# Performance work log

Measured on AMD Instinct MI355X. Metric: run time of the kernel, lower is better.

Reference implementation:

```python
import jax, jax.numpy as jnp
import numpy as np

NEG = 1e12  # matches the torch '-inf' surrogate value


def _sinusoidal_pos(seq_len, dim):
    # bert4keras-style: pe[..., 0::2] = sin, pe[..., 1::2] = cos
    pos = jnp.arange(seq_len, dtype=jnp.float32)
    i = jnp.arange(dim // 2, dtype=jnp.float32)
    freq = jnp.power(10000.0, -2.0 * i / dim)
    ang = pos[:, None] * freq[None, :]                      # [S, dim/2]
    pe = jnp.stack([jnp.sin(ang), jnp.cos(ang)], axis=-1)   # [S, dim/2, 2]
    return pe.reshape(seq_len, dim)                          # [S, dim]


def _rope(e, cos_pos, sin_pos):
    # additional_part = stack([-e[...,1::2], e[...,::2]], -1).reshape(e.shape)
    rot = jnp.stack([-e[..., 1::2], e[..., 0::2]], axis=-1).reshape(e.shape)
    return e * cos_pos + rot * sin_pos


def setup_inputs() -> dict:
    key = jax.random.key(0)
    k = jax.random.split(key, 5)
    B, S, H, inner, L = 8, 512, 768, 64, 16
    x = jax.random.normal(k[0], (B, S, H), dtype=jnp.float32)
    W1 = jax.random.normal(k[1], (H, 2 * inner), dtype=jnp.float32) * 0.02
    b1 = jnp.zeros((2 * inner,), dtype=jnp.float32)
    W2 = jax.random.normal(k[2], (H, 2 * L), dtype=jnp.float32) * 0.02
    b2 = jnp.zeros((2 * L,), dtype=jnp.float32)
    attention_mask = jnp.ones((B, S), dtype=jnp.int32)
    return {"x": x, "W1": W1, "b1": b1, "W2": W2, "b2": b2,
            "attention_mask": attention_mask}


def reference(x, W1, b1, W2, b2, attention_mask):
    B, S, H = x.shape
    inner = W1.shape[1] // 2

    t = x @ W1 + b1                                 # [B,S,2*inner]
    start_token = t[..., 0::2]                      # [B,S,inner]
    end_token = t[..., 1::2]                        # [B,S,inner]

    pe = _sinusoidal_pos(S, inner)[None]            # [1,S,inner]
    cos_pos = jnp.repeat(pe[..., 1::2], 2, axis=-1)
    sin_pos = jnp.repeat(pe[..., 0::2], 2, axis=-1)
    start_token = _rope(start_token, cos_pos, sin_pos)
    end_token = _rope(end_token, cos_pos, sin_pos)

    span_score = jnp.einsum('bmd,bnd->bmn', start_token, end_token) / (inner ** 0.5)

    typing = jnp.swapaxes(x @ W2 + b2, 1, 2) / 2.0  # [B,2L,S]

    # entity_score: [B, L, S(start), S(end)]
    entity_score = (span_score[:, None]
                    + typing[:, 0::2, None, :]
                    + typing[:, 1::2, :, None])

    m = attention_mask.astype(entity_score.dtype)
    m_row = m[:, None, :, None]                     # mask over start axis
    m_col = m[:, None, None, :]                     # mask over end axis
    entity_score = entity_score * m_row + (-NEG) * (1.0 - m_row)
    entity_score = entity_score * m_col + (-NEG) * (1.0 - m_col)

    tril = jnp.tril(jnp.ones((S, S), entity_score.dtype), k=-1)
    entity_score = entity_score - tril * NEG
    return entity_score
```

## Files before the change

kernel.cpp:

```cpp
#include <hip/hip_runtime.h>

#define NEGF 1.0e12f

constexpr int Hdim = 768;
constexpr int NC   = 160;
constexpr int ROWS = 4096;
constexpr int SEQ  = 512;
constexpr int KSPLIT = 4;

typedef __attribute__((ext_vector_type(8))) short  short8;
typedef __attribute__((ext_vector_type(4))) float  floatx4;

__device__ inline unsigned short f2bf(float f) {
    union { float f; unsigned u; } v; v.f = f;
    return (unsigned short)((v.u + 0x8000u) >> 16);
}

__global__ __launch_bounds__(256) void gemm_mfma_k(
    const float* __restrict__ x, const float* __restrict__ W1,
    const float* __restrict__ W2, float* __restrict__ partial)
{
    __shared__ __align__(16) unsigned short xs[64 * 40];
    __shared__ __align__(16) unsigned short ws[NC * 40];

    const int tid  = threadIdx.x;
    const int wave = tid >> 6;
    const int lane = tid & 63;
    const int quad = lane >> 4;
    const int nl   = lane & 15;
    const int r0   = blockIdx.x * 64;
    const int k0   = blockIdx.y * 192;

    floatx4 acc[10];
#pragma unroll
    for (int t = 0; t < 10; t++) acc[t] = (floatx4)(0.0f);

    for (int kt = 0; kt < 192; kt += 32) {
        const int kb = k0 + kt;
        {
            const int row = tid >> 2;
            const int kq  = (tid & 3) * 8;
            const float* xp = x + (size_t)(r0 + row) * Hdim + kb + kq;
            float4 v0 = *(const float4*)xp;
            float4 v1 = *(const float4*)(xp + 4);
            short8 sv;
            sv[0] = (short)f2bf(v0.x); sv[1] = (short)f2bf(v0.y);
            sv[2] = (short)f2bf(v0.z); sv[3] = (short)f2bf(v0.w);
            sv[4] = (short)f2bf(v1.x); sv[5] = (short)f2bf(v1.y);
            sv[6] = (short)f2bf(v1.z); sv[7] = (short)f2bf(v1.w);
            *(short8*)(xs + row * 40 + kq) = sv;
        }
#pragma unroll
        for (int g = 0; g < 3; g++) {
            const int c   = g * 64 + (tid & 63);
            const int kq2 = (tid >> 6) * 8;
            if (c < NC) {
                float f[8];
                if (c < 128) {
                    const float* wp = W1 + (size_t)(kb + kq2) * 128 + c;
#pragma unroll
                    for (int j = 0; j < 8; j++) f[j] = wp[j * 128];
                } else {
                    const float* wp = W2 + (size_t)(kb + kq2) * 32 + (c - 128);
#pragma unroll
                    for (int j = 0; j < 8; j++) f[j] = wp[j * 32];
                }
                short8 sv;
#pragma unroll
                for (int j = 0; j < 8; j++) sv[j] = (short)f2bf(f[j]);
                *(short8*)(ws + c * 40 + kq2) = sv;
            }
        }
        __syncthreads();

        short8 af = *(const short8*)(xs + (wave * 16 + nl) * 40 + quad * 8);
#pragma unroll
        for (int t = 0; t < 10; t++) {
            short8 bf = *(const short8*)(ws + (t * 16 + nl) * 40 + quad * 8);
            acc[t] = __builtin_amdgcn_mfma_f32_16x16x32_bf16(af, bf, acc[t], 0, 0, 0);
        }
        __syncthreads();
    }

    float* pout = partial + (size_t)blockIdx.y * ROWS * NC;
#pragma unroll
    for (int t = 0; t < 10; t++) {
#pragma unroll
        for (int r = 0; r < 4; r++) {
            pout[(size_t)(r0 + wave * 16 + quad * 4 + r) * NC + t * 16 + nl] = acc[t][r];
        }
    }
}

__global__ __launch_bounds__(256) void combine_rope_k(
    const float* __restrict__ partial, const float* __restrict__ b1,
    const float* __restrict__ b2, unsigned short* __restrict__ startbf,
    unsigned short* __restrict__ endbf, float* __restrict__ tyn,
    float* __restrict__ tym)
{
    const int tid = threadIdx.x;
    const int row = blockIdx.x * 4 + (tid >> 6);
    const int u   = tid & 63;
    const int b   = row >> 9;
    const int s   = row & 511;
    const float* p0 = partial + (size_t)row * NC;
    const size_t cstride = (size_t)ROWS * NC;

    if (u < 32) {
        const int i = u;
        float4 a0 = *(const float4*)(p0 + 4 * i);
        float4 a1 = *(const float4*)(p0 + cstride + 4 * i);
        float4 a2 = *(const float4*)(p0 + 2 * cstride + 4 * i);
        float4 a3 = *(const float4*)(p0 + 3 * cstride + 4 * i);
        float t0 = a0.x + a1.x + a2.x + a3.x + b1[4 * i + 0];
        float t1 = a0.y + a1.y + a2.y + a3.y + b1[4 * i + 1];
        float t2 = a0.z + a1.z + a2.z + a3.z + b1[4 * i + 2];
        float t3 = a0.w + a1.w + a2.w + a3.w + b1[4 * i + 3];
        float freq = __powf(10000.0f, -(float)i * (1.0f / 32.0f));
        float ang  = (float)s * freq;
        float sn, cs;
        __sincosf(ang, &sn, &cs);
        float so0 = (t0 * cs - t2 * sn) * 0.125f;
        float so1 = (t2 * cs + t0 * sn) * 0.125f;
        float eo0 = t1 * cs - t3 * sn;
        float eo1 = t3 * cs + t1 * sn;
        ushort2 sp; sp.x = f2bf(so0); sp.y = f2bf(so1);
        ushort2 ep; ep.x = f2bf(eo0); ep.y = f2bf(eo1);
        *(ushort2*)(startbf + (size_t)row * 64 + 2 * i) = sp;
        *(ushort2*)(endbf   + (size_t)row * 64 + 2 * i) = ep;
    } else {
        const int j = u - 32;
        float t = p0[128 + j] + p0[cstride + 128 + j] + p0[2 * cstride + 128 + j]
                + p0[3 * cstride + 128 + j] + b2[j];
        float v = t * 0.5f;
        const int l = j >> 1;
        if ((j & 1) == 0) tyn[((size_t)b * 16 + l) * SEQ + s] = v;
        else              tym[((size_t)b * 16 + l) * SEQ + s] = v;
    }
}

__global__ __launch_bounds__(256) void entity_k(
    const unsigned short* __restrict__ startbf, const unsigned short* __restrict__ endbf,
    const float* __restrict__ tyn, const float* __restrict__ tym,
    const int* __restrict__ amask, float* __restrict__ out)
{
    __shared__ __align__(16) unsigned short sA[64 * 72];
    __shared__ __align__(16) unsigned short sB[64 * 72];
    __shared__ float tyn_s[16 * 64];
    __shared__ float tym_s[16 * 64];
    __shared__ float mrow_s[64];
    __shared__ float mcol_s[64];

    const int tid = threadIdx.x;
    const int b   = blockIdx.z;
    const int m0  = blockIdx.y * 64;
    const int n0  = blockIdx.x * 64;

    for (int t = tid; t < 512; t += 256) {
        int row = t >> 3;
        int kq  = (t & 7) * 8;
        *(short8*)(sA + row * 72 + kq) =
            *(const short8*)(startbf + (size_t)(b * SEQ + m0 + row) * 64 + kq);
        *(short8*)(sB + row * 72 + kq) =
            *(const short8*)(endbf + (size_t)(b * SEQ + n0 + row) * 64 + kq);
    }
    for (int t = tid; t < 16 * 64; t += 256) {
        int l = t >> 6, i = t & 63;
        tym_s[t] = tym[((size_t)b * 16 + l) * SEQ + m0 + i];
        tyn_s[t] = tyn[((size_t)b * 16 + l) * SEQ + n0 + i];
    }
    if (tid < 64)       mrow_s[tid] = (float)amask[b * SEQ + m0 + tid];
    else if (tid < 128) mcol_s[tid - 64] = (float)amask[b * SEQ + n0 + (tid - 64)];
    __syncthreads();

    const int wave = tid >> 6;
    const int lane = tid & 63;
    const int quad = lane >> 4;
    const int nl   = lane & 15;

    short8 a0 = *(const short8*)(sA + (wave * 16 + nl) * 72 + quad * 8);
    short8 a1 = *(const short8*)(sA + (wave * 16 + nl) * 72 + 32 + quad * 8);

    floatx4 acc[4];
#pragma unroll
    for (int t = 0; t < 4; t++) acc[t] = (floatx4)(0.0f);
#pragma unroll
    for (int t = 0; t < 4; t++) {
        short8 bf0 = *(const short8*)(sB + (t * 16 + nl) * 72 + quad * 8);
        short8 bf1 = *(const short8*)(sB + (t * 16 + nl) * 72 + 32 + quad * 8);
        acc[t] = __builtin_amdgcn_mfma_f32_16x16x32_bf16(a0, bf0, acc[t], 0, 0, 0);
        acc[t] = __builtin_amdgcn_mfma_f32_16x16x32_bf16(a1, bf1, acc[t], 0, 0, 0);
    }

    float mr[4], radd[4];
#pragma unroll
    for (int r = 0; r < 4; r++) {
        mr[r]   = mrow_s[wave * 16 + quad * 4 + r];
        radd[r] = -NEGF * (1.0f - mr[r]);
    }
    float mc[4], cadd[4];
#pragma unroll
    for (int t = 0; t < 4; t++) {
        mc[t]   = mcol_s[t * 16 + nl];
        cadd[t] = -NEGF * (1.0f - mc[t]);
    }
    const bool lower = (m0 > n0);
    const bool diag  = (m0 == n0);
    const int  lm    = wave * 16 + quad * 4;

    for (int l = 0; l < 16; l++) {
        float tmv[4];
#pragma unroll
        for (int r = 0; r < 4; r++) tmv[r] = tym_s[l * 64 + lm + r];
        float* ob = out + ((size_t)(b * 16 + l) * SEQ + m0 + lm) * SEQ + n0;
#pragma unroll
        for (int t = 0; t < 4; t++) {
            float tnv = tyn_s[l * 64 + t * 16 + nl];
#pragma unroll
            for (int r = 0; r < 4; r++) {
                float v = acc[t][r] + tnv + tmv[r];
                v = v * mr[r] + radd[r];
                v = v * mc[t] + cadd[t];
                if (lower) v -= NEGF;
                else if (diag && (lm + r > t * 16 + nl)) v -= NEGF;
                ob[(size_t)r * SEQ + t * 16 + nl] = v;
            }
        }
    }
}

extern "C" void kernel_launch(void* const* d_in, const int* in_sizes, int n_in,
                              void* d_out, int out_size, void* d_ws, size_t ws_size,
                              hipStream_t stream) {
    const float* x     = (const float*)d_in[0];
    const float* W1    = (const float*)d_in[1];
    const float* b1    = (const float*)d_in[2];
    const float* W2    = (const float*)d_in[3];
    const float* b2    = (const float*)d_in[4];
    const int*   amask = (const int*)d_in[5];
    float* out = (float*)d_out;

    char* base = (char*)d_ws;
    float*          partial = (float*)base;
    unsigned short* startbf = (unsigned short*)(base + 10485760);
    unsigned short* endbf   = (unsigned short*)(base + 10485760 + 524288);
    float*          tyn     = (float*)(base + 10485760 + 2 * 524288);
    float*          tym     = (float*)(base + 10485760 + 2 * 524288 + 262144);

    hipLaunchKernelGGL(gemm_mfma_k, dim3(64, KSPLIT), dim3(256), 0, stream,
                       x, W1, W2, partial);
    hipLaunchKernelGGL(combine_rope_k, dim3(ROWS / 4), dim3(256), 0, stream,
                       partial, b1, b2, startbf, endbf, tyn, tym);
    hipLaunchKernelGGL(entity_k, dim3(8, 8, 8), dim3(256), 0, stream,
                       startbf, endbf, tyn, tym, amask, out);
}
```

Before: 169.7 us.

## Transpose entity MFMA tile for float4 nontemporal stores, split labels, skip lower tiles

The entity kernel swaps the MFMA operand roles so each lane holds four consecutive output columns, which lets it write each group with one 16-byte nontemporal store instead of four scalar stores. The grid is doubled so each block handles 8 of the 16 labels, and blocks whose tile lies entirely below the diagonal skip the shared-memory loads and the MFMA. The aim is to cut store-instruction count and cache pollution on this write-bound output. In exchange, each block now reloads the same operand tiles for its half of the labels, and the transposed layout makes the masking and index logic more involved.

```diff
diff --git a/kernel.cpp b/kernel.cpp
--- a/kernel.cpp
+++ b/kernel.cpp
@@ -144,87 +144,95 @@
     const float* __restrict__ tyn, const float* __restrict__ tym,
     const int* __restrict__ amask, float* __restrict__ out)
 {
-    __shared__ __align__(16) unsigned short sA[64 * 72];
-    __shared__ __align__(16) unsigned short sB[64 * 72];
-    __shared__ float tyn_s[16 * 64];
-    __shared__ float tym_s[16 * 64];
+    __shared__ __align__(16) unsigned short sE[64 * 72];
+    __shared__ __align__(16) unsigned short sS[64 * 72];
+    __shared__ float tyn_s[8 * 64];
+    __shared__ float tym_s[8 * 64];
     __shared__ float mrow_s[64];
     __shared__ float mcol_s[64];
 
     const int tid = threadIdx.x;
-    const int b   = blockIdx.z;
+    const int bz  = blockIdx.z;
+    const int b   = bz >> 1;
+    const int l0  = (bz & 1) * 8;
     const int m0  = blockIdx.y * 64;
     const int n0  = blockIdx.x * 64;
-
-    for (int t = tid; t < 512; t += 256) {
-        int row = t >> 3;
-        int kq  = (t & 7) * 8;
-        *(short8*)(sA + row * 72 + kq) =
-            *(const short8*)(startbf + (size_t)(b * SEQ + m0 + row) * 64 + kq);
-        *(short8*)(sB + row * 72 + kq) =
-            *(const short8*)(endbf + (size_t)(b * SEQ + n0 + row) * 64 + kq);
-    }
-    for (int t = tid; t < 16 * 64; t += 256) {
-        int l = t >> 6, i = t & 63;
-        tym_s[t] = tym[((size_t)b * 16 + l) * SEQ + m0 + i];
-        tyn_s[t] = tyn[((size_t)b * 16 + l) * SEQ + n0 + i];
-    }
-    if (tid < 64)       mrow_s[tid] = (float)amask[b * SEQ + m0 + tid];
-    else if (tid < 128) mcol_s[tid - 64] = (float)amask[b * SEQ + n0 + (tid - 64)];
-    __syncthreads();
-
-    const int wave = tid >> 6;
-    const int lane = tid & 63;
-    const int quad = lane >> 4;
-    const int nl   = lane & 15;
-
-    short8 a0 = *(const short8*)(sA + (wave * 16 + nl) * 72 + quad * 8);
-    short8 a1 = *(const short8*)(sA + (wave * 16 + nl) * 72 + 32 + quad * 8);
-
-    floatx4 acc[4];
-#pragma unroll
-    for (int t = 0; t < 4; t++) acc[t] = (floatx4)(0.0f);
-#pragma unroll
-    for (int t = 0; t < 4; t++) {
-        short8 bf0 = *(const short8*)(sB + (t * 16 + nl) * 72 + quad * 8);
-        short8 bf1 = *(const short8*)(sB + (t * 16 + nl) * 72 + 32 + quad * 8);
-        acc[t] = __builtin_amdgcn_mfma_f32_16x16x32_bf16(a0, bf0, acc[t], 0, 0, 0);
-        acc[t] = __builtin_amdgcn_mfma_f32_16x16x32_bf16(a1, bf1, acc[t], 0, 0, 0);
-    }
-
-    float mr[4], radd[4];
-#pragma unroll
-    for (int r = 0; r < 4; r++) {
-        mr[r]   = mrow_s[wave * 16 + quad * 4 + r];
-        radd[r] = -NEGF * (1.0f - mr[r]);
-    }
-    float mc[4], cadd[4];
-#pragma unroll
-    for (int t = 0; t < 4; t++) {
-        mc[t]   = mcol_s[t * 16 + nl];
-        cadd[t] = -NEGF * (1.0f - mc[t]);
-    }
     const bool lower = (m0 > n0);
     const bool diag  = (m0 == n0);
-    const int  lm    = wave * 16 + quad * 4;
-
-    for (int l = 0; l < 16; l++) {
-        float tmv[4];
-#pragma unroll
-        for (int r = 0; r < 4; r++) tmv[r] = tym_s[l * 64 + lm + r];
-        float* ob = out + ((size_t)(b * 16 + l) * SEQ + m0 + lm) * SEQ + n0;
+
+    if (tid < 64)       mrow_s[tid]      = (float)amask[b * SEQ + m0 + tid];
+    else if (tid < 128) mcol_s[tid - 64] = (float)amask[b * SEQ + n0 + (tid - 64)];
+
+    if (!lower) {
+        for (int t = tid; t < 512; t += 256) {
+            int row = t >> 3;
+            int kq  = (t & 7) * 8;
+            *(short8*)(sE + row * 72 + kq) =
+                *(const short8*)(endbf + (size_t)(b * SEQ + n0 + row) * 64 + kq);
+            *(short8*)(sS + row * 72 + kq) =
+                *(const short8*)(startbf + (size_t)(b * SEQ + m0 + row) * 64 + kq);
+        }
+        for (int t = tid; t < 8 * 64; t += 256) {
+            int l = t >> 6, i = t & 63;
+            tym_s[t] = tym[((size_t)b * 16 + l0 + l) * SEQ + m0 + i];
+            tyn_s[t] = tyn[((size_t)b * 16 + l0 + l) * SEQ + n0 + i];
+        }
+    }
+    __syncthreads();
+
+    const int wave  = tid >> 6;
+    const int lane  = tid & 63;
+    const int quad  = lane >> 4;
+    const int nl    = lane & 15;
+    const int nloc0 = wave * 16 + quad * 4;
+
+    floatx4 acc[4];
+#pragma unroll
+    for (int t = 0; t < 4; t++) acc[t] = (floatx4)(0.0f);
+
+    if (!lower) {
+        short8 a0 = *(const short8*)(sE + (wave * 16 + nl) * 72 + quad * 8);
+        short8 a1 = *(const short8*)(sE + (wave * 16 + nl) * 72 + 32 + quad * 8);
 #pragma unroll
         for (int t = 0; t < 4; t++) {
-            float tnv = tyn_s[l * 64 + t * 16 + nl];
+            short8 bf0 = *(const short8*)(sS + (t * 16 + nl) * 72 + quad * 8);
+            short8 bf1 = *(const short8*)(sS + (t * 16 + nl) * 72 + 32 + quad * 8);
+            acc[t] = __builtin_amdgcn_mfma_f32_16x16x32_bf16(a0, bf0, acc[t], 0, 0, 0);
+            acc[t] = __builtin_amdgcn_mfma_f32_16x16x32_bf16(a1, bf1, acc[t], 0, 0, 0);
+        }
+    }
+
+    float mc4[4], cadd4[4];
+#pragma unroll
+    for (int r = 0; r < 4; r++) {
+        mc4[r]   = mcol_s[nloc0 + r];
+        cadd4[r] = -NEGF * (1.0f - mc4[r]);
+    }
+    float mrt[4], raddt[4];
+#pragma unroll
+    for (int t = 0; t < 4; t++) {
+        mrt[t]   = mrow_s[t * 16 + nl];
+        raddt[t] = -NEGF * (1.0f - mrt[t]);
+    }
+
+    for (int l = 0; l < 8; l++) {
+        floatx4 tn4 = (floatx4)(0.0f);
+        if (!lower) tn4 = *(const floatx4*)(tyn_s + l * 64 + nloc0);
+        float* op = out + (((size_t)(b * 16 + l0 + l)) * SEQ + m0) * SEQ + n0 + nloc0;
+#pragma unroll
+        for (int t = 0; t < 4; t++) {
+            float tm = lower ? 0.0f : tym_s[l * 64 + t * 16 + nl];
+            floatx4 v;
 #pragma unroll
             for (int r = 0; r < 4; r++) {
-                float v = acc[t][r] + tnv + tmv[r];
-                v = v * mr[r] + radd[r];
-                v = v * mc[t] + cadd[t];
-                if (lower) v -= NEGF;
-                else if (diag && (lm + r > t * 16 + nl)) v -= NEGF;
-                ob[(size_t)r * SEQ + t * 16 + nl] = v;
+                float x = acc[t][r] + tn4[r] + tm;
+                x = x * mrt[t] + raddt[t];
+                x = x * mc4[r] + cadd4[r];
+                if (lower) x -= NEGF;
+                else if (diag && (t * 16 + nl) > (nloc0 + r)) x -= NEGF;
+                v[r] = x;
             }
+            __builtin_nontemporal_store(v, (floatx4*)(op + (size_t)(t * 16 + nl) * SEQ));
         }
     }
 }
@@ -251,6 +259,6 @@
                        x, W1, W2, partial);
     hipLaunchKernelGGL(combine_rope_k, dim3(ROWS / 4), dim3(256), 0, stream,
                        partial, b1, b2, startbf, endbf, tyn, tym);
-    hipLaunchKernelGGL(entity_k, dim3(8, 8, 8), dim3(256), 0, stream,
+    hipLaunchKernelGGL(entity_k, dim3(8, 8, 16), dim3(256), 0, stream,
                        startbf, endbf, tyn, tym, amask, out);
 }
```

Result: slower. 190.5 us (+12.3%).

## Split entity kernel into span GEMM and vectorized broadcast-write kernel

Applied to the files above, without the earlier changes.

Splits the fused entity kernel into two. span_k computes only the upper-triangular span tiles and writes them to a workspace buffer that reuses the partial area. bcast_k then reads each span row once and writes all 16 label planes with contiguous float4 stores, zeroing the lower-triangular span terms before applying masks. The goal is to replace the strided scalar output stores of the old kernel with coalesced vector writes, at the cost of an extra launch and a round trip of the span matrix through memory.

```diff
diff --git a/kernel.cpp b/kernel.cpp
--- a/kernel.cpp
+++ b/kernel.cpp
@@ -139,23 +139,19 @@
     }
 }
 
-__global__ __launch_bounds__(256) void entity_k(
+__global__ __launch_bounds__(256) void span_k(
     const unsigned short* __restrict__ startbf, const unsigned short* __restrict__ endbf,
-    const float* __restrict__ tyn, const float* __restrict__ tym,
-    const int* __restrict__ amask, float* __restrict__ out)
-{
+    float* __restrict__ span)
+{
+    const int b  = blockIdx.z;
+    const int m0 = blockIdx.y * 64;
+    const int n0 = blockIdx.x * 64;
+    if (m0 > n0) return;
+
     __shared__ __align__(16) unsigned short sA[64 * 72];
     __shared__ __align__(16) unsigned short sB[64 * 72];
-    __shared__ float tyn_s[16 * 64];
-    __shared__ float tym_s[16 * 64];
-    __shared__ float mrow_s[64];
-    __shared__ float mcol_s[64];
 
     const int tid = threadIdx.x;
-    const int b   = blockIdx.z;
-    const int m0  = blockIdx.y * 64;
-    const int n0  = blockIdx.x * 64;
-
     for (int t = tid; t < 512; t += 256) {
         int row = t >> 3;
         int kq  = (t & 7) * 8;
@@ -164,13 +160,6 @@
         *(short8*)(sB + row * 72 + kq) =
             *(const short8*)(endbf + (size_t)(b * SEQ + n0 + row) * 64 + kq);
     }
-    for (int t = tid; t < 16 * 64; t += 256) {
-        int l = t >> 6, i = t & 63;
-        tym_s[t] = tym[((size_t)b * 16 + l) * SEQ + m0 + i];
-        tyn_s[t] = tyn[((size_t)b * 16 + l) * SEQ + n0 + i];
-    }
-    if (tid < 64)       mrow_s[tid] = (float)amask[b * SEQ + m0 + tid];
-    else if (tid < 128) mcol_s[tid - 64] = (float)amask[b * SEQ + n0 + (tid - 64)];
     __syncthreads();
 
     const int wave = tid >> 6;
@@ -192,39 +181,76 @@
         acc[t] = __builtin_amdgcn_mfma_f32_16x16x32_bf16(a1, bf1, acc[t], 0, 0, 0);
     }
 
-    float mr[4], radd[4];
-#pragma unroll
-    for (int r = 0; r < 4; r++) {
-        mr[r]   = mrow_s[wave * 16 + quad * 4 + r];
-        radd[r] = -NEGF * (1.0f - mr[r]);
-    }
-    float mc[4], cadd[4];
 #pragma unroll
     for (int t = 0; t < 4; t++) {
-        mc[t]   = mcol_s[t * 16 + nl];
-        cadd[t] = -NEGF * (1.0f - mc[t]);
-    }
-    const bool lower = (m0 > n0);
-    const bool diag  = (m0 == n0);
-    const int  lm    = wave * 16 + quad * 4;
-
-    for (int l = 0; l < 16; l++) {
-        float tmv[4];
-#pragma unroll
-        for (int r = 0; r < 4; r++) tmv[r] = tym_s[l * 64 + lm + r];
-        float* ob = out + ((size_t)(b * 16 + l) * SEQ + m0 + lm) * SEQ + n0;
-#pragma unroll
-        for (int t = 0; t < 4; t++) {
-            float tnv = tyn_s[l * 64 + t * 16 + nl];
-#pragma unroll
-            for (int r = 0; r < 4; r++) {
-                float v = acc[t][r] + tnv + tmv[r];
-                v = v * mr[r] + radd[r];
-                v = v * mc[t] + cadd[t];
-                if (lower) v -= NEGF;
-                else if (diag && (lm + r > t * 16 + nl)) v -= NEGF;
-                ob[(size_t)r * SEQ + t * 16 + nl] = v;
+#pragma unroll
+        for (int r = 0; r < 4; r++) {
+            span[((size_t)(b * SEQ) + m0 + wave * 16 + quad * 4 + r) * SEQ
+                 + n0 + t * 16 + nl] = acc[t][r];
+        }
+    }
+}
+
+__global__ __launch_bounds__(256) void bcast_k(
+    const float* __restrict__ span, const float* __restrict__ tyn,
+    const float* __restrict__ tym, const int* __restrict__ amask,
+    float* __restrict__ out)
+{
+    __shared__ float tyn_s[8 * SEQ];
+    __shared__ float tym_s[64];
+
+    const int tid = threadIdx.x;
+    const int m0  = blockIdx.x * 8;
+    const int l0  = blockIdx.y * 8;
+    const int b   = blockIdx.z;
+
+    for (int t = tid; t < 8 * SEQ / 4; t += 256)
+        ((floatx4*)tyn_s)[t] = ((const floatx4*)(tyn + ((size_t)b * 16 + l0) * SEQ))[t];
+    if (tid < 64) {
+        int l = tid >> 3, r = tid & 7;
+        tym_s[tid] = tym[((size_t)b * 16 + l0 + l) * SEQ + m0 + r];
+    }
+
+    const int r  = tid >> 5;
+    const int cb = (tid & 31) * 4;
+    const int m  = m0 + r;
+    const float mr   = (float)amask[b * SEQ + m];
+    const float radd = -NEGF * (1.0f - mr);
+
+    float spanz[16], mc[16], cadd2[16];
+#pragma unroll
+    for (int q = 0; q < 4; q++) {
+        floatx4 s4 = *(const floatx4*)(span + ((size_t)b * SEQ + m) * SEQ + cb + q * 128);
+        int4 mk = *(const int4*)(amask + b * SEQ + cb + q * 128);
+        const int* mki = (const int*)&mk;
+#pragma unroll
+        for (int e = 0; e < 4; e++) {
+            const int j = q * 4 + e;
+            const int n = cb + q * 128 + e;
+            mc[j] = (float)mki[e];
+            float ca = -NEGF * (1.0f - mc[j]);
+            cadd2[j] = (n < m) ? (ca - NEGF) : ca;
+            spanz[j] = (n >= m) ? s4[e] : 0.0f;
+        }
+    }
+    __syncthreads();
+
+    for (int l = 0; l < 8; l++) {
+        const float tm = tym_s[l * 8 + r];
+        float* orow = out + (((size_t)(b * 16 + l0 + l)) * SEQ + m) * SEQ;
+#pragma unroll
+        for (int q = 0; q < 4; q++) {
+            floatx4 t4 = *(const floatx4*)(tyn_s + l * SEQ + cb + q * 128);
+            floatx4 v;
+#pragma unroll
+            for (int e = 0; e < 4; e++) {
+                const int j = q * 4 + e;
+                float x = spanz[j] + t4[e] + tm;
+                x = x * mr + radd;
+                x = x * mc[j] + cadd2[j];
+                v[e] = x;
             }
+            *(floatx4*)(orow + cb + q * 128) = v;
         }
     }
 }
@@ -246,11 +272,14 @@
     unsigned short* endbf   = (unsigned short*)(base + 10485760 + 524288);
     float*          tyn     = (float*)(base + 10485760 + 2 * 524288);
     float*          tym     = (float*)(base + 10485760 + 2 * 524288 + 262144);
+    float*          span    = partial;
 
     hipLaunchKernelGGL(gemm_mfma_k, dim3(64, KSPLIT), dim3(256), 0, stream,
                        x, W1, W2, partial);
     hipLaunchKernelGGL(combine_rope_k, dim3(ROWS / 4), dim3(256), 0, stream,
                        partial, b1, b2, startbf, endbf, tyn, tym);
-    hipLaunchKernelGGL(entity_k, dim3(8, 8, 8), dim3(256), 0, stream,
-                       startbf, endbf, tyn, tym, amask, out);
-}
+    hipLaunchKernelGGL(span_k, dim3(8, 8, 8), dim3(256), 0, stream,
+                       startbf, endbf, span);
+    hipLaunchKernelGGL(bcast_k, dim3(64, 2, 8), dim3(256), 0, stream,
+                       span, tyn, tym, amask, out);
+}
```

After: 175.3 us. 1.03x slower.

## Fuse split-K GEMM with RoPE combine and restructure entity kernel by row strips

Applied to the files above, without the earlier changes.

The projection GEMM now does its K-split inside one block, with two wave pairs each covering half of K. Their partials are reduced through shared memory and RoPE plus typing are applied in the same kernel. This removes the global partial buffer and the separate combine launch. The entity kernel now computes a 16-row by full-512-column span strip per block, skips MFMA tiles entirely below the diagonal, and stages typing in LDS. It then writes 8 labels with float4 row-contiguous stores. In exchange the GEMM runs on only 256 blocks, and the entity kernel carries more registers and LDS per block.

```diff
diff --git a/kernel.cpp b/kernel.cpp
--- a/kernel.cpp
+++ b/kernel.cpp
@@ -3,12 +3,10 @@
 #define NEGF 1.0e12f
 
 constexpr int Hdim = 768;
-constexpr int NC   = 160;
-constexpr int ROWS = 4096;
 constexpr int SEQ  = 512;
-constexpr int KSPLIT = 4;
 
 typedef __attribute__((ext_vector_type(8))) short  short8;
+typedef __attribute__((ext_vector_type(4))) short  short4v;
 typedef __attribute__((ext_vector_type(4))) float  floatx4;
 
 __device__ inline unsigned short f2bf(float f) {
@@ -16,106 +14,108 @@
     return (unsigned short)((v.u + 0x8000u) >> 16);
 }
 
-__global__ __launch_bounds__(256) void gemm_mfma_k(
+__global__ __launch_bounds__(256) void gemm_rope_k(
     const float* __restrict__ x, const float* __restrict__ W1,
-    const float* __restrict__ W2, float* __restrict__ partial)
+    const float* __restrict__ W2, const float* __restrict__ b1,
+    const float* __restrict__ b2, unsigned short* __restrict__ startbf,
+    unsigned short* __restrict__ endbf, float* __restrict__ tyn,
+    float* __restrict__ tym)
 {
-    __shared__ __align__(16) unsigned short xs[64 * 40];
-    __shared__ __align__(16) unsigned short ws[NC * 40];
+    __shared__ __align__(16) char smem[28160];
+    unsigned short* xs = (unsigned short*)smem;
+    unsigned short* ws = xs + 2 * 16 * 40;
+    float* tacc = (float*)smem;
 
     const int tid  = threadIdx.x;
+    const int r0   = blockIdx.x * 16;
     const int wave = tid >> 6;
     const int lane = tid & 63;
     const int quad = lane >> 4;
     const int nl   = lane & 15;
-    const int r0   = blockIdx.x * 64;
-    const int k0   = blockIdx.y * 192;
-
-    floatx4 acc[10];
-#pragma unroll
-    for (int t = 0; t < 10; t++) acc[t] = (floatx4)(0.0f);
-
-    for (int kt = 0; kt < 192; kt += 32) {
-        const int kb = k0 + kt;
+    const int ch   = wave & 1;
+    const int kh   = wave >> 1;
+
+    floatx4 acc[5];
+#pragma unroll
+    for (int t = 0; t < 5; t++) acc[t] = (floatx4)(0.0f);
+
+    for (int kt = 0; kt < 384; kt += 32) {
         {
-            const int row = tid >> 2;
-            const int kq  = (tid & 3) * 8;
-            const float* xp = x + (size_t)(r0 + row) * Hdim + kb + kq;
-            float4 v0 = *(const float4*)xp;
-            float4 v1 = *(const float4*)(xp + 4);
-            short8 sv;
-            sv[0] = (short)f2bf(v0.x); sv[1] = (short)f2bf(v0.y);
-            sv[2] = (short)f2bf(v0.z); sv[3] = (short)f2bf(v0.w);
-            sv[4] = (short)f2bf(v1.x); sv[5] = (short)f2bf(v1.y);
-            sv[6] = (short)f2bf(v1.z); sv[7] = (short)f2bf(v1.w);
-            *(short8*)(xs + row * 40 + kq) = sv;
-        }
-#pragma unroll
-        for (int g = 0; g < 3; g++) {
-            const int c   = g * 64 + (tid & 63);
-            const int kq2 = (tid >> 6) * 8;
-            if (c < NC) {
-                float f[8];
-                if (c < 128) {
-                    const float* wp = W1 + (size_t)(kb + kq2) * 128 + c;
-#pragma unroll
-                    for (int j = 0; j < 8; j++) f[j] = wp[j * 128];
-                } else {
-                    const float* wp = W2 + (size_t)(kb + kq2) * 32 + (c - 128);
-#pragma unroll
-                    for (int j = 0; j < 8; j++) f[j] = wp[j * 32];
+            const int khs = tid >> 7;
+            const int row = (tid >> 3) & 15;
+            const int kq  = (tid & 7) * 4;
+            const float* xp = x + (size_t)(r0 + row) * Hdim + khs * 384 + kt + kq;
+            float4 v = *(const float4*)xp;
+            short4v sv;
+            sv[0] = (short)f2bf(v.x); sv[1] = (short)f2bf(v.y);
+            sv[2] = (short)f2bf(v.z); sv[3] = (short)f2bf(v.w);
+            *(short4v*)(xs + khs * 640 + row * 40 + kq) = sv;
+        }
+        {
+            const int khs = tid >> 7;
+            const int sub = tid & 127;
+            const int kq2 = (sub >> 6) * 8;
+#pragma unroll
+            for (int g = 0; g < 3; g++) {
+                const int c = g * 64 + (sub & 63);
+                if (c < 160) {
+#pragma unroll
+                    for (int h = 0; h < 2; h++) {
+                        const int ko = kq2 + h * 16;
+                        const int kg = khs * 384 + kt + ko;
+                        float f[8];
+                        if (c < 128) {
+                            const float* wp = W1 + (size_t)kg * 128 + c;
+#pragma unroll
+                            for (int j = 0; j < 8; j++) f[j] = wp[j * 128];
+                        } else {
+                            const float* wp = W2 + (size_t)kg * 32 + (c - 128);
+#pragma unroll
+                            for (int j = 0; j < 8; j++) f[j] = wp[j * 32];
+                        }
+                        short8 sv;
+#pragma unroll
+                        for (int j = 0; j < 8; j++) sv[j] = (short)f2bf(f[j]);
+                        *(short8*)(ws + khs * 6400 + c * 40 + ko) = sv;
+                    }
                 }
-                short8 sv;
-#pragma unroll
-                for (int j = 0; j < 8; j++) sv[j] = (short)f2bf(f[j]);
-                *(short8*)(ws + c * 40 + kq2) = sv;
             }
         }
         __syncthreads();
 
-        short8 af = *(const short8*)(xs + (wave * 16 + nl) * 40 + quad * 8);
-#pragma unroll
-        for (int t = 0; t < 10; t++) {
-            short8 bf = *(const short8*)(ws + (t * 16 + nl) * 40 + quad * 8);
+        short8 af = *(const short8*)(xs + kh * 640 + nl * 40 + quad * 8);
+#pragma unroll
+        for (int t = 0; t < 5; t++) {
+            short8 bf = *(const short8*)(ws + kh * 6400 + (ch * 80 + t * 16 + nl) * 40 + quad * 8);
             acc[t] = __builtin_amdgcn_mfma_f32_16x16x32_bf16(af, bf, acc[t], 0, 0, 0);
         }
         __syncthreads();
     }
 
-    float* pout = partial + (size_t)blockIdx.y * ROWS * NC;
-#pragma unroll
-    for (int t = 0; t < 10; t++) {
-#pragma unroll
-        for (int r = 0; r < 4; r++) {
-            pout[(size_t)(r0 + wave * 16 + quad * 4 + r) * NC + t * 16 + nl] = acc[t][r];
-        }
-    }
-}
-
-__global__ __launch_bounds__(256) void combine_rope_k(
-    const float* __restrict__ partial, const float* __restrict__ b1,
-    const float* __restrict__ b2, unsigned short* __restrict__ startbf,
-    unsigned short* __restrict__ endbf, float* __restrict__ tyn,
-    float* __restrict__ tym)
-{
-    const int tid = threadIdx.x;
-    const int row = blockIdx.x * 4 + (tid >> 6);
-    const int u   = tid & 63;
-    const int b   = row >> 9;
-    const int s   = row & 511;
-    const float* p0 = partial + (size_t)row * NC;
-    const size_t cstride = (size_t)ROWS * NC;
-
-    if (u < 32) {
-        const int i = u;
-        float4 a0 = *(const float4*)(p0 + 4 * i);
-        float4 a1 = *(const float4*)(p0 + cstride + 4 * i);
-        float4 a2 = *(const float4*)(p0 + 2 * cstride + 4 * i);
-        float4 a3 = *(const float4*)(p0 + 3 * cstride + 4 * i);
-        float t0 = a0.x + a1.x + a2.x + a3.x + b1[4 * i + 0];
-        float t1 = a0.y + a1.y + a2.y + a3.y + b1[4 * i + 1];
-        float t2 = a0.z + a1.z + a2.z + a3.z + b1[4 * i + 2];
-        float t3 = a0.w + a1.w + a2.w + a3.w + b1[4 * i + 3];
+#pragma unroll
+    for (int t = 0; t < 5; t++)
+#pragma unroll
+        for (int r = 0; r < 4; r++)
+            tacc[kh * (16 * 164) + (quad * 4 + r) * 164 + ch * 80 + t * 16 + nl] = acc[t][r];
+    __syncthreads();
+
+    const int row = tid >> 4;
+    const int uu  = tid & 15;
+    const int R   = r0 + row;
+    const int bb  = R >> 9;
+    const int s   = R & 511;
+    const float* t0p = tacc + row * 164;
+    const float* t1p = tacc + 16 * 164 + row * 164;
+#pragma unroll
+    for (int ii = 0; ii < 2; ii++) {
+        const int i = uu + ii * 16;
+        floatx4 a  = *(const floatx4*)(t0p + 4 * i);
+        floatx4 c  = *(const floatx4*)(t1p + 4 * i);
+        floatx4 bv = *(const floatx4*)(b1 + 4 * i);
+        float t0 = a[0] + c[0] + bv[0];
+        float t1 = a[1] + c[1] + bv[1];
+        float t2 = a[2] + c[2] + bv[2];
+        float t3 = a[3] + c[3] + bv[3];
         float freq = __powf(10000.0f, -(float)i * (1.0f / 32.0f));
         float ang  = (float)s * freq;
         float sn, cs;
@@ -124,107 +124,111 @@
         float so1 = (t2 * cs + t0 * sn) * 0.125f;
         float eo0 = t1 * cs - t3 * sn;
         float eo1 = t3 * cs + t1 * sn;
-        ushort2 sp; sp.x = f2bf(so0); sp.y = f2bf(so1);
-        ushort2 ep; ep.x = f2bf(eo0); ep.y = f2bf(eo1);
-        *(ushort2*)(startbf + (size_t)row * 64 + 2 * i) = sp;
-        *(ushort2*)(endbf   + (size_t)row * 64 + 2 * i) = ep;
-    } else {
-        const int j = u - 32;
-        float t = p0[128 + j] + p0[cstride + 128 + j] + p0[2 * cstride + 128 + j]
-                + p0[3 * cstride + 128 + j] + b2[j];
+        ushort2 sp2; sp2.x = f2bf(so0); sp2.y = f2bf(so1);
+        ushort2 ep2; ep2.x = f2bf(eo0); ep2.y = f2bf(eo1);
+        *(ushort2*)(startbf + (size_t)R * 64 + 2 * i) = sp2;
+        *(ushort2*)(endbf   + (size_t)R * 64 + 2 * i) = ep2;
+    }
+#pragma unroll
+    for (int jj = 0; jj < 2; jj++) {
+        const int j = uu + jj * 16;
+        float t = t0p[128 + j] + t1p[128 + j] + b2[j];
         float v = t * 0.5f;
         const int l = j >> 1;
-        if ((j & 1) == 0) tyn[((size_t)b * 16 + l) * SEQ + s] = v;
-        else              tym[((size_t)b * 16 + l) * SEQ + s] = v;
-    }
-}
-
-__global__ __launch_bounds__(256) void entity_k(
+        if ((j & 1) == 0) tyn[((size_t)bb * 16 + l) * SEQ + s] = v;
+        else              tym[((size_t)bb * 16 + l) * SEQ + s] = v;
+    }
+}
+
+__global__ __launch_bounds__(256, 2) void entity_fused_k(
     const unsigned short* __restrict__ startbf, const unsigned short* __restrict__ endbf,
     const float* __restrict__ tyn, const float* __restrict__ tym,
     const int* __restrict__ amask, float* __restrict__ out)
 {
-    __shared__ __align__(16) unsigned short sA[64 * 72];
-    __shared__ __align__(16) unsigned short sB[64 * 72];
-    __shared__ float tyn_s[16 * 64];
-    __shared__ float tym_s[16 * 64];
-    __shared__ float mrow_s[64];
-    __shared__ float mcol_s[64];
-
-    const int tid = threadIdx.x;
-    const int b   = blockIdx.z;
-    const int m0  = blockIdx.y * 64;
-    const int n0  = blockIdx.x * 64;
-
-    for (int t = tid; t < 512; t += 256) {
-        int row = t >> 3;
-        int kq  = (t & 7) * 8;
-        *(short8*)(sA + row * 72 + kq) =
-            *(const short8*)(startbf + (size_t)(b * SEQ + m0 + row) * 64 + kq);
-        *(short8*)(sB + row * 72 + kq) =
-            *(const short8*)(endbf + (size_t)(b * SEQ + n0 + row) * 64 + kq);
-    }
-    for (int t = tid; t < 16 * 64; t += 256) {
-        int l = t >> 6, i = t & 63;
-        tym_s[t] = tym[((size_t)b * 16 + l) * SEQ + m0 + i];
-        tyn_s[t] = tyn[((size_t)b * 16 + l) * SEQ + n0 + i];
-    }
-    if (tid < 64)       mrow_s[tid] = (float)amask[b * SEQ + m0 + tid];
-    else if (tid < 128) mcol_s[tid - 64] = (float)amask[b * SEQ + n0 + (tid - 64)];
-    __syncthreads();
-
+    __shared__ __align__(16) float span_s[16 * 516];
+    __shared__ __align__(16) float tyn_s[8 * SEQ];
+    __shared__ float tym_s[8 * 16];
+
+    const int tid  = threadIdx.x;
+    const int m0   = blockIdx.x * 16;
+    const int lh   = blockIdx.y;
+    const int b    = blockIdx.z;
     const int wave = tid >> 6;
     const int lane = tid & 63;
     const int quad = lane >> 4;
     const int nl   = lane & 15;
 
-    short8 a0 = *(const short8*)(sA + (wave * 16 + nl) * 72 + quad * 8);
-    short8 a1 = *(const short8*)(sA + (wave * 16 + nl) * 72 + 32 + quad * 8);
-
-    floatx4 acc[4];
-#pragma unroll
-    for (int t = 0; t < 4; t++) acc[t] = (floatx4)(0.0f);
-#pragma unroll
-    for (int t = 0; t < 4; t++) {
-        short8 bf0 = *(const short8*)(sB + (t * 16 + nl) * 72 + quad * 8);
-        short8 bf1 = *(const short8*)(sB + (t * 16 + nl) * 72 + 32 + quad * 8);
-        acc[t] = __builtin_amdgcn_mfma_f32_16x16x32_bf16(a0, bf0, acc[t], 0, 0, 0);
-        acc[t] = __builtin_amdgcn_mfma_f32_16x16x32_bf16(a1, bf1, acc[t], 0, 0, 0);
-    }
-
-    float mr[4], radd[4];
-#pragma unroll
-    for (int r = 0; r < 4; r++) {
-        mr[r]   = mrow_s[wave * 16 + quad * 4 + r];
-        radd[r] = -NEGF * (1.0f - mr[r]);
-    }
-    float mc[4], cadd[4];
-#pragma unroll
-    for (int t = 0; t < 4; t++) {
-        mc[t]   = mcol_s[t * 16 + nl];
-        cadd[t] = -NEGF * (1.0f - mc[t]);
-    }
-    const bool lower = (m0 > n0);
-    const bool diag  = (m0 == n0);
-    const int  lm    = wave * 16 + quad * 4;
-
-    for (int l = 0; l < 16; l++) {
-        float tmv[4];
-#pragma unroll
-        for (int r = 0; r < 4; r++) tmv[r] = tym_s[l * 64 + lm + r];
-        float* ob = out + ((size_t)(b * 16 + l) * SEQ + m0 + lm) * SEQ + n0;
-#pragma unroll
-        for (int t = 0; t < 4; t++) {
-            float tnv = tyn_s[l * 64 + t * 16 + nl];
-#pragma unroll
-            for (int r = 0; r < 4; r++) {
-                float v = acc[t][r] + tnv + tmv[r];
-                v = v * mr[r] + radd[r];
-                v = v * mc[t] + cadd[t];
-                if (lower) v -= NEGF;
-                else if (diag && (lm + r > t * 16 + nl)) v -= NEGF;
-                ob[(size_t)r * SEQ + t * 16 + nl] = v;
+    const unsigned short* ap = startbf + ((size_t)(b * SEQ + m0 + nl)) * 64 + quad * 8;
+    short8 a0 = *(const short8*)ap;
+    short8 a1 = *(const short8*)(ap + 32);
+
+    floatx4 acc[8];
+#pragma unroll
+    for (int t = 0; t < 8; t++) acc[t] = (floatx4)(0.0f);
+#pragma unroll
+    for (int t = 0; t < 8; t++) {
+        if (wave * 128 + t * 16 + 15 >= m0) {
+            const unsigned short* ep =
+                endbf + ((size_t)(b * SEQ + wave * 128 + t * 16 + nl)) * 64 + quad * 8;
+            short8 bf0 = *(const short8*)ep;
+            short8 bf1 = *(const short8*)(ep + 32);
+            acc[t] = __builtin_amdgcn_mfma_f32_16x16x32_bf16(a0, bf0, acc[t], 0, 0, 0);
+            acc[t] = __builtin_amdgcn_mfma_f32_16x16x32_bf16(a1, bf1, acc[t], 0, 0, 0);
+        }
+    }
+
+    {
+        const floatx4* src = (const floatx4*)(tyn + ((size_t)b * 16 + lh * 8) * SEQ);
+        for (int t = tid; t < 8 * SEQ / 4; t += 256) ((floatx4*)tyn_s)[t] = src[t];
+        if (tid < 128) {
+            const int l = tid >> 4, r = tid & 15;
+            tym_s[tid] = tym[((size_t)b * 16 + lh * 8 + l) * SEQ + m0 + r];
+        }
+    }
+#pragma unroll
+    for (int t = 0; t < 8; t++)
+#pragma unroll
+        for (int r = 0; r < 4; r++)
+            span_s[(quad * 4 + r) * 516 + wave * 128 + t * 16 + nl] = acc[t][r];
+    __syncthreads();
+
+    const int row = tid >> 4;
+    const int uu  = tid & 15;
+    const int m   = m0 + row;
+    const float mr   = (float)amask[b * SEQ + m];
+    const float radd = -NEGF * (1.0f - mr);
+
+    floatx4 spanz[8], mcv[8], caddv[8];
+#pragma unroll
+    for (int q = 0; q < 8; q++) {
+        spanz[q] = *(const floatx4*)(span_s + row * 516 + uu * 4 + q * 64);
+        const int4 mk = *(const int4*)(amask + b * SEQ + uu * 4 + q * 64);
+        const int mki[4] = {mk.x, mk.y, mk.z, mk.w};
+#pragma unroll
+        for (int e = 0; e < 4; e++) {
+            const int n = uu * 4 + q * 64 + e;
+            float mc = (float)mki[e];
+            mcv[q][e] = mc;
+            float ca = -NEGF * (1.0f - mc);
+            caddv[q][e] = (n < m) ? (ca - NEGF) : ca;
+        }
+    }
+
+    for (int l = 0; l < 8; l++) {
+        const float tm = tym_s[l * 16 + row];
+        float* orow = out + (((size_t)(b * 16 + lh * 8 + l)) * SEQ + m) * SEQ;
+#pragma unroll
+        for (int q = 0; q < 8; q++) {
+            floatx4 t4 = *(const floatx4*)(tyn_s + l * SEQ + uu * 4 + q * 64);
+            floatx4 v;
+#pragma unroll
+            for (int e = 0; e < 4; e++) {
+                float xv = spanz[q][e] + t4[e] + tm;
+                xv = xv * mr + radd;
+                xv = xv * mcv[q][e] + caddv[q][e];
+                v[e] = xv;
             }
+            *(floatx4*)(orow + uu * 4 + q * 64) = v;
         }
     }
 }
@@ -241,16 +245,13 @@
     float* out = (float*)d_out;
 
     char* base = (char*)d_ws;
-    float*          partial = (float*)base;
-    unsigned short* startbf = (unsigned short*)(base + 10485760);
-    unsigned short* endbf   = (unsigned short*)(base + 10485760 + 524288);
-    float*          tyn     = (float*)(base + 10485760 + 2 * 524288);
-    float*          tym     = (float*)(base + 10485760 + 2 * 524288 + 262144);
-
-    hipLaunchKernelGGL(gemm_mfma_k, dim3(64, KSPLIT), dim3(256), 0, stream,
-                       x, W1, W2, partial);
-    hipLaunchKernelGGL(combine_rope_k, dim3(ROWS / 4), dim3(256), 0, stream,
-                       partial, b1, b2, startbf, endbf, tyn, tym);
-    hipLaunchKernelGGL(entity_k, dim3(8, 8, 8), dim3(256), 0, stream,
+    unsigned short* startbf = (unsigned short*)base;
+    unsigned short* endbf   = (unsigned short*)(base + 524288);
+    float*          tyn     = (float*)(base + 1048576);
+    float*          tym     = (float*)(base + 1048576 + 262144);
+
+    hipLaunchKernelGGL(gemm_rope_k, dim3(256), dim3(256), 0, stream,
+                       x, W1, W2, b1, b2, startbf, endbf, tyn, tym);
+    hipLaunchKernelGGL(entity_fused_k, dim3(32, 2, 8), dim3(256), 0, stream,
                        startbf, endbf, tyn, tym, amask, out);
 }
```

Measured after the change: 177.3 us. +4.5%, slower.
